# Optimization experiments

Measured on AMD Instinct MI355X. Metric: run time of the kernel, lower is better.

The kernel has to match this reference:

```python
import jax, jax.numpy as jnp
import numpy as np

N = 20000   # nodes
E = 320000  # edges (avg degree 16)
H = 4       # heads
C = 128     # per-head / output channels (concat=False -> mean over heads)
IN = 2      # init_channels (TSP coords)
NEG_SLOPE = 0.2


def setup_inputs() -> dict:
    key = jax.random.key(0)
    ks = jax.random.split(key, 32)
    s = 0.1
    def W(k, shape):
        return (jax.random.normal(k, shape, jnp.float32) * s)
    inp = {
        "x": jax.random.normal(ks[0], (N, IN), jnp.float32),
        "edge_index": jax.random.randint(ks[1], (2, E), 0, N, jnp.int32),
        "edge_attr": jax.random.uniform(ks[2], (E, 1), jnp.float32),
    }
    i = 3
    for b in range(2):  # two parallel GATBlocks
        inp[f"Wsrc{b}"]  = W(ks[i+0], (IN, H * C))
        inp[f"bsrc{b}"]  = jnp.zeros((H * C,), jnp.float32)
        inp[f"Wdst{b}"]  = W(ks[i+1], (IN, H * C))
        inp[f"bdst{b}"]  = jnp.zeros((H * C,), jnp.float32)
        inp[f"Wedge{b}"] = W(ks[i+2], (1, H * C))
        inp[f"att{b}"]   = W(ks[i+3], (H, C))
        inp[f"bias{b}"]  = jnp.zeros((C,), jnp.float32)
        inp[f"Wres{b}"]  = W(ks[i+4], (IN, C))  # SkipConnection projection (2 -> 128)
        i += 5
    inp["Wfuse"] = W(ks[i], (2 * C, C))
    inp["bfuse"] = jnp.zeros((C,), jnp.float32)
    return inp


def _gat_block(x, src, dst, ea, Wsrc, bsrc, Wdst, bdst, Wedge, att, bias, Wres):
    # GATv2Conv (concat=False) + ReLU + residual projection
    xs = (x @ Wsrc + bsrc).reshape(N, H, C)   # lin_l (source / message)
    xd = (x @ Wdst + bdst).reshape(N, H, C)   # lin_r (target)
    ee = (ea @ Wedge).reshape(-1, H, C)       # lin_edge
    e = jax.nn.leaky_relu(xs[src] + xd[dst] + ee, NEG_SLOPE)  # [Etot,H,C]
    logits = jnp.einsum('ehc,hc->eh', e, att)                 # [Etot,H]
    # segment softmax over incoming edges of each target node
    m = jax.ops.segment_max(logits, dst, num_segments=N)
    m = jnp.where(jnp.isfinite(m), m, 0.0)
    p = jnp.exp(logits - m[dst])
    denom = jax.ops.segment_sum(p, dst, num_segments=N)
    alpha = p / (denom[dst] + 1e-16)                          # [Etot,H]
    agg = jax.ops.segment_sum(xs[src] * alpha[:, :, None], dst, num_segments=N)
    out = agg.mean(axis=1) + bias                             # concat=False: mean heads
    return jax.nn.relu(out) + x @ Wres                        # ReLU then skip add


def reference(x, edge_index, edge_attr,
              Wsrc0, bsrc0, Wdst0, bdst0, Wedge0, att0, bias0, Wres0,
              Wsrc1, bsrc1, Wdst1, bdst1, Wedge1, att1, bias1, Wres1,
              Wfuse, bfuse):
    src, dst = edge_index[0], edge_index[1]
    # PyG default add_self_loops=True, fill_value='mean' for edge_attr
    loop = jnp.arange(N, dtype=src.dtype)
    src_a = jnp.concatenate([src, loop])
    dst_a = jnp.concatenate([dst, loop])
    mean_attr = jnp.mean(edge_attr, axis=0, keepdims=True)
    ea = jnp.concatenate([edge_attr, jnp.broadcast_to(mean_attr, (N, 1))], axis=0)

    h0 = _gat_block(x, src_a, dst_a, ea, Wsrc0, bsrc0, Wdst0, bdst0, Wedge0, att0, bias0, Wres0)
    h1 = _gat_block(x, src_a, dst_a, ea, Wsrc1, bsrc1, Wdst1, bdst1, Wedge1, att1, bias1, Wres1)
    xc = jnp.concatenate([h0, h1], axis=-1)       # [N, 2C]
    return jax.nn.relu(xc @ Wfuse + bfuse)        # [N, C]
```

## Files before the change

kernel.cpp:

```cpp
#include <hip/hip_runtime.h>

#define HH 4
#define CC 128
#define NPB 16

static inline size_t roundup256(size_t x) { return (x + 255) & ~(size_t)255; }

__global__ __launch_bounds__(256) void prep_kernel(
    const int* __restrict__ ei, const float* __restrict__ eattr,
    float* __restrict__ meansum, float* __restrict__ Lin, int* __restrict__ cnt,
    const float* __restrict__ Wsrc0, const float* __restrict__ bsrc0,
    const float* __restrict__ Wdst0, const float* __restrict__ bdst0,
    const float* __restrict__ Wedge0, const float* __restrict__ att0,
    const float* __restrict__ Wsrc1, const float* __restrict__ bsrc1,
    const float* __restrict__ Wdst1, const float* __restrict__ bdst1,
    const float* __restrict__ Wedge1, const float* __restrict__ att1,
    float* __restrict__ packed, int E)
{
    int tid = blockIdx.x * 256 + threadIdx.x;
    int lane = threadIdx.x & 63, wid = threadIdx.x >> 6;
    float s = 0.f;
    if (tid < E) {
        atomicAdd(&cnt[ei[E + tid]], 1);
        s = eattr[tid];
    }
    #pragma unroll
    for (int off = 32; off > 0; off >>= 1) s += __shfl_down(s, off, 64);
    __shared__ float wsum[4];
    if (lane == 0) wsum[wid] = s;
    __syncthreads();
    if (threadIdx.x == 0)
        atomicAdd(meansum, wsum[0] + wsum[1] + wsum[2] + wsum[3]);

    if (blockIdx.x < 4) {
        int b = tid >> 9;
        int hc = tid & 511;
        int c = hc & 127;
        int h = hc >> 7;
        int bh = b * 4 + h;
        const float* Ws = b ? Wsrc1 : Wsrc0;
        const float* bs = b ? bsrc1 : bsrc0;
        const float* Wd = b ? Wdst1 : Wdst0;
        const float* bd = b ? bdst1 : bdst0;
        const float* We = b ? Wedge1 : Wedge0;
        const float* at = b ? att1 : att0;
        float A = Ws[hc], B = Ws[512 + hc];
        float C = Wd[hc], D = Wd[512 + hc];
        float Ec = We[hc];
        float F = bs[hc] + bd[hc];
        float a = at[hc];
        float4* r = (float4*)(packed + ((size_t)(bh * 128 + c)) * 8);
        r[0] = make_float4(A, B, C, D);
        r[1] = make_float4(Ec, F, 0.4f * a, 0.f);
        float sa = 0.6f * a;
        float vals[6] = {sa * A, sa * B, sa * C, sa * D, sa * Ec, sa * F};
        #pragma unroll
        for (int k = 0; k < 6; ++k) {
            float v = vals[k];
            #pragma unroll
            for (int off = 32; off > 0; off >>= 1) v += __shfl_down(v, off, 64);
            vals[k] = v;
        }
        __shared__ float Ls[4][6];
        if (lane == 0) {
            #pragma unroll
            for (int k = 0; k < 6; ++k) Ls[wid][k] = vals[k];
        }
        __syncthreads();
        if (threadIdx.x < 12) {
            int w2 = threadIdx.x / 6;
            int k = threadIdx.x % 6;
            int bhg = blockIdx.x * 2 + w2;
            Lin[bhg * 6 + k] = Ls[w2 * 2][k] + Ls[w2 * 2 + 1][k];
        }
    }
}

__global__ __launch_bounds__(1024) void scan_kernel(const int* __restrict__ cnt,
                                                    int* __restrict__ rowptr,
                                                    int* __restrict__ cur, int N) {
    const int CH = 32;
    int t = threadIdx.x;
    int base = t * CH;
    int local[CH];
    int s = 0;
    #pragma unroll
    for (int i = 0; i < CH; ++i) {
        int idx = base + i;
        int v = (idx < N) ? cnt[idx] + 1 : 0;
        local[i] = s;
        s += v;
    }
    __shared__ int sums[1024];
    sums[t] = s;
    __syncthreads();
    for (int off = 1; off < 1024; off <<= 1) {
        int v = (t >= off) ? sums[t - off] : 0;
        __syncthreads();
        sums[t] += v;
        __syncthreads();
    }
    int excl = sums[t] - s;
    #pragma unroll
    for (int i = 0; i < CH; ++i) {
        int idx = base + i;
        if (idx < N) {
            int v = excl + local[i];
            rowptr[idx] = v;
            cur[idx] = v;
        }
    }
    if (t == 1023) rowptr[N] = excl + s;
}

__global__ __launch_bounds__(256) void scatter_kernel(
    const int* __restrict__ ei, const float* __restrict__ x,
    const float* __restrict__ eattr, const float* __restrict__ meansum,
    int* __restrict__ cur, float4* __restrict__ ed4, float* __restrict__ ea1,
    int N, int E) {
    int e = blockIdx.x * 256 + threadIdx.x;
    int Etot = E + N;
    if (e >= Etot) return;
    int src, dst;
    float ea;
    if (e < E) { src = ei[e]; dst = ei[E + e]; ea = eattr[e]; }
    else       { src = e - E; dst = src; ea = meansum[0] / (float)E; }
    int pos = atomicAdd(&cur[dst], 1);
    const float2* x2 = (const float2*)x;
    float2 xs = x2[src];
    float2 xd = x2[dst];
    ed4[pos] = make_float4(xs.x, xs.y, xd.x, xd.y);
    ea1[pos] = ea;
}

__global__ __launch_bounds__(256) void logits_kernel(
    const float4* __restrict__ ed4,
    const float* __restrict__ ea1,
    const float* __restrict__ Lin,
    const float4* __restrict__ pw,
    float* __restrict__ p8, int EtotPad, int nchunks)
{
    int blk = blockIdx.x;
    int bh = blk / nchunks;
    int chunk = blk - bh * nchunks;
    int t = threadIdx.x;
    int iA = chunk * 512 + t;
    int iB = iA + 256;
    float4 eA = ed4[iA], eB = ed4[iB];
    float aA = ea1[iA], aB = ea1[iB];

    const float4* wp = pw + (size_t)bh * 256;
    float a0 = 0.f, a1 = 0.f;
    #pragma unroll 8
    for (int c = 0; c < 128; ++c) {
        float4 w0 = wp[2 * c];
        float4 w1 = wp[2 * c + 1];
        float uA = fmaf(w0.x, eA.x,
                   fmaf(w0.y, eA.y,
                   fmaf(w0.z, eA.z,
                   fmaf(w0.w, eA.w,
                   fmaf(w1.x, aA, w1.y)))));
        float uB = fmaf(w0.x, eB.x,
                   fmaf(w0.y, eB.y,
                   fmaf(w0.z, eB.z,
                   fmaf(w0.w, eB.w,
                   fmaf(w1.x, aB, w1.y)))));
        a0 = fmaf(w1.z, __builtin_fabsf(uA), a0);
        a1 = fmaf(w1.z, __builtin_fabsf(uB), a1);
    }

    const float* Lp = Lin + bh * 6;
    float lgA = fmaf(Lp[0], eA.x, fmaf(Lp[1], eA.y, fmaf(Lp[2], eA.z,
                fmaf(Lp[3], eA.w, fmaf(Lp[4], aA, Lp[5]))))) + a0;
    float lgB = fmaf(Lp[0], eB.x, fmaf(Lp[1], eB.y, fmaf(Lp[2], eB.z,
                fmaf(Lp[3], eB.w, fmaf(Lp[4], aB, Lp[5]))))) + a1;
    float* plane = p8 + (size_t)bh * EtotPad;
    plane[iA] = __expf(lgA);
    plane[iB] = __expf(lgB);
}

__global__ __launch_bounds__(256) void nodeS_kernel(
    const int* __restrict__ rowptr, const float4* __restrict__ ed4,
    const float* __restrict__ p8, float* __restrict__ S, int N, int EtotPad)
{
    int t = threadIdx.x;
    int g = t >> 3, bh = t & 7;
    int n = blockIdx.x * 32 + g;
    if (n >= N) return;
    int beg = rowptr[n], end = rowptr[n + 1];
    const float* plane = p8 + (size_t)bh * EtotPad;
    float s0 = 0.f, s1 = 0.f, sb = 0.f;
    for (int i = beg; i < end; ++i) {
        float4 ed = ed4[i];
        float p = plane[i];
        s0 = fmaf(p, ed.x, s0);
        s1 = fmaf(p, ed.y, s1);
        sb += p;
    }
    float* Sp = S + (size_t)n * 24 + bh * 3;
    Sp[0] = s0;
    Sp[1] = s1;
    Sp[2] = sb;
}

__global__ __launch_bounds__(256) void node_kernel(
    const float* __restrict__ x,
    const float* __restrict__ S,
    const float* __restrict__ Wsrc0, const float* __restrict__ bsrc0,
    const float* __restrict__ bias0, const float* __restrict__ Wres0,
    const float* __restrict__ Wsrc1, const float* __restrict__ bsrc1,
    const float* __restrict__ bias1, const float* __restrict__ Wres1,
    const float* __restrict__ Wfuse, const float* __restrict__ bfuse,
    float* __restrict__ out, int N)
{
    __shared__ __align__(16) float hbuf[NPB][2 * CC];
    int t = threadIdx.x;
    int c = t & (CC - 1);
    int half = t >> 7;
    int n0 = blockIdx.x * NPB;

    float w00[HH], w01[HH], wb0[HH], w10[HH], w11[HH], wb1[HH];
    #pragma unroll
    for (int h = 0; h < HH; ++h) {
        w00[h] = Wsrc0[h * CC + c];
        w01[h] = Wsrc0[512 + h * CC + c];
        wb0[h] = bsrc0[h * CC + c];
        w10[h] = Wsrc1[h * CC + c];
        w11[h] = Wsrc1[512 + h * CC + c];
        wb1[h] = bsrc1[h * CC + c];
    }
    float bi0 = bias0[c], bi1 = bias1[c];
    float r00 = Wres0[c], r01 = Wres0[CC + c];
    float r10 = Wres1[c], r11 = Wres1[CC + c];

    for (int ni = half; ni < NPB; ni += 2) {
        int n = n0 + ni;
        if (n < N) {
            float x0 = x[2 * n], x1 = x[2 * n + 1];
            const float4* Sp4 = (const float4*)(S + (size_t)n * 24);
            float4 q0 = Sp4[0], q1 = Sp4[1], q2 = Sp4[2];
            float4 q3 = Sp4[3], q4 = Sp4[4], q5 = Sp4[5];
            float h0v, h1v;
            {
                float s0[HH] = {q0.x, q0.w, q1.z, q2.y};
                float s1[HH] = {q0.y, q1.x, q1.w, q2.z};
                float sb[HH] = {q0.z, q1.y, q2.x, q2.w};
                float acc = 0.f;
                #pragma unroll
                for (int h = 0; h < HH; ++h) {
                    float num = fmaf(w00[h], s0[h], fmaf(w01[h], s1[h], wb0[h] * sb[h]));
                    acc += num / (sb[h] + 1e-16f);
                }
                float o = fmaxf(acc * 0.25f + bi0, 0.f);
                h0v = o + x0 * r00 + x1 * r01;
            }
            {
                float s0[HH] = {q3.x, q3.w, q4.z, q5.y};
                float s1[HH] = {q3.y, q4.x, q4.w, q5.z};
                float sb[HH] = {q3.z, q4.y, q5.x, q5.w};
                float acc = 0.f;
                #pragma unroll
                for (int h = 0; h < HH; ++h) {
                    float num = fmaf(w10[h], s0[h], fmaf(w11[h], s1[h], wb1[h] * sb[h]));
                    acc += num / (sb[h] + 1e-16f);
                }
                float o = fmaxf(acc * 0.25f + bi1, 0.f);
                h1v = o + x0 * r10 + x1 * r11;
            }
            hbuf[ni][c] = h0v;
            hbuf[ni][CC + c] = h1v;
        }
    }
    __syncthreads();

    int c2 = (t & 63) * 2;
    int grp = t >> 6;
    float accx[4], accy[4];
    float bfx = bfuse[c2], bfy = bfuse[c2 + 1];
    #pragma unroll
    for (int j = 0; j < 4; ++j) { accx[j] = bfx; accy[j] = bfy; }

    for (int i = 0; i < 2 * CC; i += 4) {
        float2 w0 = *(const float2*)&Wfuse[(i + 0) * CC + c2];
        float2 w1 = *(const float2*)&Wfuse[(i + 1) * CC + c2];
        float2 w2 = *(const float2*)&Wfuse[(i + 2) * CC + c2];
        float2 w3 = *(const float2*)&Wfuse[(i + 3) * CC + c2];
        #pragma unroll
        for (int j = 0; j < 4; ++j) {
            int ni = grp * 4 + j;
            float4 hv = *reinterpret_cast<const float4*>(&hbuf[ni][i]);
            accx[j] = fmaf(hv.x, w0.x, fmaf(hv.y, w1.x,
                      fmaf(hv.z, w2.x, fmaf(hv.w, w3.x, accx[j]))));
            accy[j] = fmaf(hv.x, w0.y, fmaf(hv.y, w1.y,
                      fmaf(hv.z, w2.y, fmaf(hv.w, w3.y, accy[j]))));
        }
    }
    #pragma unroll
    for (int j = 0; j < 4; ++j) {
        int n = n0 + grp * 4 + j;
        if (n < N) {
            float2 o = make_float2(fmaxf(accx[j], 0.f), fmaxf(accy[j], 0.f));
            *(float2*)&out[n * CC + c2] = o;
        }
    }
}

extern "C" void kernel_launch(void* const* d_in, const int* in_sizes, int n_in,
                              void* d_out, int out_size, void* d_ws, size_t ws_size,
                              hipStream_t stream) {
    const float* x      = (const float*)d_in[0];
    const int*   ei     = (const int*)d_in[1];
    const float* eattr  = (const float*)d_in[2];
    const float* Wsrc0  = (const float*)d_in[3];
    const float* bsrc0  = (const float*)d_in[4];
    const float* Wdst0  = (const float*)d_in[5];
    const float* bdst0  = (const float*)d_in[6];
    const float* Wedge0 = (const float*)d_in[7];
    const float* att0   = (const float*)d_in[8];
    const float* bias0  = (const float*)d_in[9];
    const float* Wres0  = (const float*)d_in[10];
    const float* Wsrc1  = (const float*)d_in[11];
    const float* bsrc1  = (const float*)d_in[12];
    const float* Wdst1  = (const float*)d_in[13];
    const float* bdst1  = (const float*)d_in[14];
    const float* Wedge1 = (const float*)d_in[15];
    const float* att1   = (const float*)d_in[16];
    const float* bias1  = (const float*)d_in[17];
    const float* Wres1  = (const float*)d_in[18];
    const float* Wfuse  = (const float*)d_in[19];
    const float* bfuse  = (const float*)d_in[20];
    float* out = (float*)d_out;

    int N = in_sizes[0] / 2;
    int E = in_sizes[1] / 2;
    int Etot = E + N;
    int EtotPad = (Etot + 511) & ~511;

    size_t off = 0;
    float* meansum = (float*)((char*)d_ws + off);  off += 256;
    int*   cnt     = (int*)((char*)d_ws + off);    off += roundup256((size_t)N * sizeof(int));
    size_t zero_bytes = off;
    float* Lin     = (float*)((char*)d_ws + off);  off += 256;
    int*   cur     = (int*)((char*)d_ws + off);    off += roundup256((size_t)N * sizeof(int));
    int*   rowptr  = (int*)((char*)d_ws + off);    off += roundup256((size_t)(N + 1) * sizeof(int));
    float* packed  = (float*)((char*)d_ws + off);  off += roundup256(8 * 128 * 8 * sizeof(float));
    float4* ed4    = (float4*)((char*)d_ws + off); off += roundup256((size_t)EtotPad * sizeof(float4));
    float* ea1     = (float*)((char*)d_ws + off);  off += roundup256((size_t)EtotPad * sizeof(float));
    float* p8      = (float*)((char*)d_ws + off);  off += roundup256((size_t)EtotPad * 8 * sizeof(float));
    float* S       = (float*)((char*)d_ws + off);  off += roundup256((size_t)24 * N * sizeof(float));

    hipMemsetAsync(d_ws, 0, zero_bytes, stream);

    prep_kernel<<<(E + 255) / 256, 256, 0, stream>>>(
        ei, eattr, meansum, Lin, cnt,
        Wsrc0, bsrc0, Wdst0, bdst0, Wedge0, att0,
        Wsrc1, bsrc1, Wdst1, bdst1, Wedge1, att1,
        packed, E);

    scan_kernel<<<1, 1024, 0, stream>>>(cnt, rowptr, cur, N);

    scatter_kernel<<<(Etot + 255) / 256, 256, 0, stream>>>(
        ei, x, eattr, meansum, cur, ed4, ea1, N, E);

    int nchunks = EtotPad / 512;
    logits_kernel<<<8 * nchunks, 256, 0, stream>>>(
        ed4, ea1, Lin, (const float4*)packed, p8, EtotPad, nchunks);

    nodeS_kernel<<<(N + 31) / 32, 256, 0, stream>>>(rowptr, ed4, p8, S, N, EtotPad);

    node_kernel<<<(N + NPB - 1) / NPB, 256, 0, stream>>>(
        x, S,
        Wsrc0, bsrc0, bias0, Wres0,
        Wsrc1, bsrc1, bias1, Wres1,
        Wfuse, bfuse, out, N);
}
```

Measured before the change: 197.1 us.

## Use bf16 MFMA for fuse GEMM with prepacked Wfuse and pre-normalized sums

The final 256->128 fuse projection in node_kernel moves from scalar FP32 FMAs to bf16 MFMA 16x16x32 instructions. Wfuse is converted to bf16 and packed into the MFMA B-operand layout inside prep_kernel. Node features are staged in shared memory as bf16, and each block now handles 64 nodes with 512 threads. The softmax normalization divide moves into nodeS_kernel as a single reciprocal per node-head, which removes the per-head divisions from node_kernel. Rounding activations and weights to bf16 lowers accuracy.

```diff
diff --git a/kernel.cpp b/kernel.cpp
--- a/kernel.cpp
+++ b/kernel.cpp
@@ -2,9 +2,18 @@
 
 #define HH 4
 #define CC 128
-#define NPB 16
+#define NPB 64
+
+typedef __attribute__((ext_vector_type(8))) short short8v;
+typedef __attribute__((ext_vector_type(4))) float f32x4;
 
 static inline size_t roundup256(size_t x) { return (x + 255) & ~(size_t)255; }
+
+static __device__ __forceinline__ unsigned short f2bf(float f) {
+    unsigned int u = __float_as_uint(f);
+    unsigned int r = (u + 0x7FFFu + ((u >> 16) & 1u)) >> 16;
+    return (unsigned short)r;
+}
 
 __global__ __launch_bounds__(256) void prep_kernel(
     const int* __restrict__ ei, const float* __restrict__ eattr,
@@ -15,7 +24,8 @@
     const float* __restrict__ Wsrc1, const float* __restrict__ bsrc1,
     const float* __restrict__ Wdst1, const float* __restrict__ bdst1,
     const float* __restrict__ Wedge1, const float* __restrict__ att1,
-    float* __restrict__ packed, int E)
+    const float* __restrict__ Wfuse,
+    float* __restrict__ packed, unsigned short* __restrict__ pwB, int E)
 {
     int tid = blockIdx.x * 256 + threadIdx.x;
     int lane = threadIdx.x & 63, wid = threadIdx.x >> 6;
@@ -74,6 +84,21 @@
             Lin[bhg * 6 + k] = Ls[w2 * 2][k] + Ls[w2 * 2 + 1][k];
         }
     }
+
+    if (blockIdx.x < 16) {
+        int ct = tid >> 9;
+        int kc = (tid >> 6) & 7;
+        int l  = tid & 63;
+        int c = ct * 16 + (l & 15);
+        int kb = kc * 32 + (l >> 4) * 8;
+        unsigned short v[8];
+        #pragma unroll
+        for (int j = 0; j < 8; ++j)
+            v[j] = f2bf(Wfuse[(kb + j) * CC + c]);
+        unsigned short* dst = pwB + (size_t)tid * 8;
+        #pragma unroll
+        for (int j = 0; j < 8; ++j) dst[j] = v[j];
+    }
 }
 
 __global__ __launch_bounds__(1024) void scan_kernel(const int* __restrict__ cnt,
@@ -197,26 +222,27 @@
         s1 = fmaf(p, ed.y, s1);
         sb += p;
     }
+    float rin = 1.f / (sb + 1e-16f);
     float* Sp = S + (size_t)n * 24 + bh * 3;
-    Sp[0] = s0;
-    Sp[1] = s1;
-    Sp[2] = sb;
-}
-
-__global__ __launch_bounds__(256) void node_kernel(
+    Sp[0] = s0 * rin;
+    Sp[1] = s1 * rin;
+    Sp[2] = sb * rin;
+}
+
+__global__ __launch_bounds__(512) void node_kernel(
     const float* __restrict__ x,
     const float* __restrict__ S,
     const float* __restrict__ Wsrc0, const float* __restrict__ bsrc0,
     const float* __restrict__ bias0, const float* __restrict__ Wres0,
     const float* __restrict__ Wsrc1, const float* __restrict__ bsrc1,
     const float* __restrict__ bias1, const float* __restrict__ Wres1,
-    const float* __restrict__ Wfuse, const float* __restrict__ bfuse,
+    const unsigned short* __restrict__ pwB, const float* __restrict__ bfuse,
     float* __restrict__ out, int N)
 {
-    __shared__ __align__(16) float hbuf[NPB][2 * CC];
+    __shared__ __align__(16) unsigned short hb[NPB][264];
     int t = threadIdx.x;
     int c = t & (CC - 1);
-    int half = t >> 7;
+    int quarter = t >> 7;
     int n0 = blockIdx.x * NPB;
 
     float w00[HH], w01[HH], wb0[HH], w10[HH], w11[HH], wb1[HH];
@@ -233,7 +259,7 @@
     float r00 = Wres0[c], r01 = Wres0[CC + c];
     float r10 = Wres1[c], r11 = Wres1[CC + c];
 
-    for (int ni = half; ni < NPB; ni += 2) {
+    for (int ni = quarter; ni < NPB; ni += 4) {
         int n = n0 + ni;
         if (n < N) {
             float x0 = x[2 * n], x1 = x[2 * n + 1];
@@ -247,10 +273,8 @@
                 float sb[HH] = {q0.z, q1.y, q2.x, q2.w};
                 float acc = 0.f;
                 #pragma unroll
-                for (int h = 0; h < HH; ++h) {
-                    float num = fmaf(w00[h], s0[h], fmaf(w01[h], s1[h], wb0[h] * sb[h]));
-                    acc += num / (sb[h] + 1e-16f);
-                }
+                for (int h = 0; h < HH; ++h)
+                    acc += fmaf(w00[h], s0[h], fmaf(w01[h], s1[h], wb0[h] * sb[h]));
                 float o = fmaxf(acc * 0.25f + bi0, 0.f);
                 h0v = o + x0 * r00 + x1 * r01;
             }
@@ -260,47 +284,44 @@
                 float sb[HH] = {q3.z, q4.y, q5.x, q5.w};
                 float acc = 0.f;
                 #pragma unroll
-                for (int h = 0; h < HH; ++h) {
-                    float num = fmaf(w10[h], s0[h], fmaf(w11[h], s1[h], wb1[h] * sb[h]));
-                    acc += num / (sb[h] + 1e-16f);
-                }
+                for (int h = 0; h < HH; ++h)
+                    acc += fmaf(w10[h], s0[h], fmaf(w11[h], s1[h], wb1[h] * sb[h]));
                 float o = fmaxf(acc * 0.25f + bi1, 0.f);
                 h1v = o + x0 * r10 + x1 * r11;
             }
-            hbuf[ni][c] = h0v;
-            hbuf[ni][CC + c] = h1v;
+            hb[ni][c] = f2bf(h0v);
+            hb[ni][CC + c] = f2bf(h1v);
         }
     }
     __syncthreads();
 
-    int c2 = (t & 63) * 2;
-    int grp = t >> 6;
-    float accx[4], accy[4];
-    float bfx = bfuse[c2], bfy = bfuse[c2 + 1];
-    #pragma unroll
-    for (int j = 0; j < 4; ++j) { accx[j] = bfx; accy[j] = bfy; }
-
-    for (int i = 0; i < 2 * CC; i += 4) {
-        float2 w0 = *(const float2*)&Wfuse[(i + 0) * CC + c2];
-        float2 w1 = *(const float2*)&Wfuse[(i + 1) * CC + c2];
-        float2 w2 = *(const float2*)&Wfuse[(i + 2) * CC + c2];
-        float2 w3 = *(const float2*)&Wfuse[(i + 3) * CC + c2];
+    int w = t >> 6;
+    int l = t & 63;
+    int nt = w & 3;
+    int cthalf = w >> 2;
+    int row = nt * 16 + (l & 15);
+
+    short8v a[8];
+    #pragma unroll
+    for (int kc = 0; kc < 8; ++kc)
+        a[kc] = *reinterpret_cast<const short8v*>(&hb[row][kc * 32 + (l >> 4) * 8]);
+
+    const short8v* pB = reinterpret_cast<const short8v*>(pwB);
+    #pragma unroll
+    for (int ci = 0; ci < 4; ++ci) {
+        int ct = cthalf * 4 + ci;
+        f32x4 acc = {0.f, 0.f, 0.f, 0.f};
+        #pragma unroll
+        for (int kc = 0; kc < 8; ++kc) {
+            short8v b = pB[(ct * 8 + kc) * 64 + l];
+            acc = __builtin_amdgcn_mfma_f32_16x16x32_bf16(a[kc], b, acc, 0, 0, 0);
+        }
+        int ch = ct * 16 + (l & 15);
+        float bi = bfuse[ch];
         #pragma unroll
         for (int j = 0; j < 4; ++j) {
-            int ni = grp * 4 + j;
-            float4 hv = *reinterpret_cast<const float4*>(&hbuf[ni][i]);
-            accx[j] = fmaf(hv.x, w0.x, fmaf(hv.y, w1.x,
-                      fmaf(hv.z, w2.x, fmaf(hv.w, w3.x, accx[j]))));
-            accy[j] = fmaf(hv.x, w0.y, fmaf(hv.y, w1.y,
-                      fmaf(hv.z, w2.y, fmaf(hv.w, w3.y, accy[j]))));
-        }
-    }
-    #pragma unroll
-    for (int j = 0; j < 4; ++j) {
-        int n = n0 + grp * 4 + j;
-        if (n < N) {
-            float2 o = make_float2(fmaxf(accx[j], 0.f), fmaxf(accy[j], 0.f));
-            *(float2*)&out[n * CC + c2] = o;
+            int n = n0 + nt * 16 + (l >> 4) * 4 + j;
+            if (n < N) out[(size_t)n * CC + ch] = fmaxf(acc[j] + bi, 0.f);
         }
     }
 }
@@ -344,6 +365,8 @@
     int*   cur     = (int*)((char*)d_ws + off);    off += roundup256((size_t)N * sizeof(int));
     int*   rowptr  = (int*)((char*)d_ws + off);    off += roundup256((size_t)(N + 1) * sizeof(int));
     float* packed  = (float*)((char*)d_ws + off);  off += roundup256(8 * 128 * 8 * sizeof(float));
+    unsigned short* pwB = (unsigned short*)((char*)d_ws + off);
+                                                   off += roundup256(8 * 8 * 64 * 8 * sizeof(unsigned short));
     float4* ed4    = (float4*)((char*)d_ws + off); off += roundup256((size_t)EtotPad * sizeof(float4));
     float* ea1     = (float*)((char*)d_ws + off);  off += roundup256((size_t)EtotPad * sizeof(float));
     float* p8      = (float*)((char*)d_ws + off);  off += roundup256((size_t)EtotPad * 8 * sizeof(float));
@@ -355,7 +378,7 @@
         ei, eattr, meansum, Lin, cnt,
         Wsrc0, bsrc0, Wdst0, bdst0, Wedge0, att0,
         Wsrc1, bsrc1, Wdst1, bdst1, Wedge1, att1,
-        packed, E);
+        Wfuse, packed, pwB, E);
 
     scan_kernel<<<1, 1024, 0, stream>>>(cnt, rowptr, cur, N);
 
@@ -368,9 +391,9 @@
 
     nodeS_kernel<<<(N + 31) / 32, 256, 0, stream>>>(rowptr, ed4, p8, S, N, EtotPad);
 
-    node_kernel<<<(N + NPB - 1) / NPB, 256, 0, stream>>>(
+    node_kernel<<<(N + NPB - 1) / NPB, 512, 0, stream>>>(
         x, S,
         Wsrc0, bsrc0, bias0, Wres0,
         Wsrc1, bsrc1, bias1, Wres1,
-        Wfuse, bfuse, out, N);
-}
+        pwB, bfuse, out, N);
+}
```

Result: faster. 170.0 us (-13.8%).
